# Kernel optimization log

Measured on AMD Instinct MI355X. Metric: run time of the kernel, lower is better.

## Reference

```python
import jax, jax.numpy as jnp
import numpy as np

K = 32  # k-th nearest neighbor (excluding self), matches KDistanceDetector(k=32)


def setup_inputs() -> dict:
    key = jax.random.key(0)
    B, D = 16384, 128
    images = jax.random.normal(key, (B, D), dtype=jnp.float32)
    return {"images": images}


def reference(images):
    # model is identity: vision_features = images, shape [B, D]
    x = images
    # torch.cdist p=2 with mm path: sq dists via gram matrix
    sq_norms = jnp.sum(x * x, axis=1)                      # [B]
    sq = sq_norms[:, None] + sq_norms[None, :] - 2.0 * (x @ x.T)  # [B, B]
    sq = jnp.maximum(sq, 0.0)
    B = x.shape[0]
    # Mask out the diagonal (self-distance). Original removes it and views
    # [B, B-1]; setting it to +inf before sorting yields the identical k-th
    # smallest value (inf sorts last), and keeps sqrt grads clean.
    diag = jnp.eye(B, dtype=bool)
    sq = jnp.where(diag, jnp.inf, sq)
    d = jnp.sqrt(sq)                                       # [B, B]
    a = jnp.sort(d, axis=1)                                # full per-row sort, as in original
    return a[:, K]                                         # [B]
```

## Files before the change

kernel.cpp:

```cpp
#include <hip/hip_runtime.h>


typedef unsigned short u16;
typedef unsigned int   u32;
typedef __attribute__((ext_vector_type(8))) u16    ushort8;
typedef __attribute__((ext_vector_type(8))) __bf16 bf16x8;
typedef __attribute__((ext_vector_type(4))) float  f32x4;
typedef __attribute__((ext_vector_type(4))) u32    u32x4;

#define NB   16384
#define ND   128
#define NSEG 32
#define SCAP 12
#define NTH  33
#define ZWH  (-2.62f)
#define NEGF (-3.0e38f)
#define POSF ( 3.0e38f)

#define OFF_X    ((size_t)0)
#define OFF_NORM (OFF_X    + (size_t)NB * ND * 2)
#define OFF_TACC (OFF_NORM + (size_t)NB * 4)
#define OFF_XBAR (OFF_TACC + (size_t)NB * 4)
#define OFF_SCAL (OFF_XBAR + 512)
#define OFF_CNTS (OFF_SCAL + 256)
#define OFF_CAND (OFF_CNTS + (size_t)NB * NSEG * 4)

static __device__ __forceinline__ u16 f2bf(float f) {
  u32 u = __float_as_uint(f);
  u32 r = u + 0x7FFFu + ((u >> 16) & 1u);
  return (u16)(r >> 16);
}
static __device__ __forceinline__ float bf2f(u16 h) {
  return __uint_as_float(((u32)h) << 16);
}

#if defined(__has_builtin)
#if __has_builtin(__builtin_amdgcn_global_load_lds)
#define HAVE_GLDS 1
#endif
#endif

static __device__ __forceinline__ void stage16(const u16* gsrc_lane,
                                               u16* lds_base, int l) {
#ifdef HAVE_GLDS
  __builtin_amdgcn_global_load_lds(
      (const __attribute__((address_space(1))) void*)gsrc_lane,
      (__attribute__((address_space(3))) void*)lds_base, 16, 0, 0);
#else
  *(ushort8*)(lds_base + l * 8) = *(const ushort8*)gsrc_lane;
#endif
}
static __device__ __forceinline__ void stage4(const float* gsrc_lane,
                                              float* lds_base, int l) {
#ifdef HAVE_GLDS
  __builtin_amdgcn_global_load_lds(
      (const __attribute__((address_space(1))) void*)gsrc_lane,
      (__attribute__((address_space(3))) void*)lds_base, 4, 0, 0);
#else
  lds_base[l] = *gsrc_lane;
#endif
}

__global__ void k_prep(const float* __restrict__ x, u16* __restrict__ X,
                       float* __restrict__ norms, float* xbar, float* scal) {
  if (blockIdx.x == 0) {
    int tt = threadIdx.x;
    if (tt < 128) xbar[tt] = 0.f;
    if (tt < 2)   scal[tt] = 0.f;
  }
  int w = threadIdx.x >> 6, l = threadIdx.x & 63;
  int r = blockIdx.x * 4 + w;
  const float2* xr2 = (const float2*)(x + (size_t)r * ND);
  float2 a = xr2[l];
  u16 h0 = f2bf(a.x), h1 = f2bf(a.y);
  float b0 = bf2f(h0), b1 = bf2f(h1);
  float n = b0 * b0 + b1 * b1;
#pragma unroll
  for (int off = 1; off < 64; off <<= 1) n += __shfl_xor(n, off, 64);
  *(u32*)(X + (size_t)r * ND + 2 * l) = (u32)h0 | ((u32)h1 << 16);
  if (l == 0) norms[r] = n;
}

__global__ void k_stats(const u16* __restrict__ X, const float* __restrict__ norms,
                        float* xbar, float* scal) {
  __shared__ float xs[16][128];
  __shared__ float red1[256], red2[256];
  int t = threadIdx.x;
  int cg = t & 15;
  int rs = t >> 4;
  int rbase = blockIdx.x * 256;
  float s[8] = {0.f, 0.f, 0.f, 0.f, 0.f, 0.f, 0.f, 0.f};
  for (int rr = 0; rr < 16; ++rr) {
    int row = rbase + rs + rr * 16;
    ushort8 v = *(const ushort8*)(X + (size_t)row * ND + cg * 8);
#pragma unroll
    for (int u = 0; u < 8; ++u) s[u] += bf2f(v[u]);
  }
#pragma unroll
  for (int u = 0; u < 8; ++u) xs[rs][cg * 8 + u] = s[u];
  float ln = norms[rbase + t];
  red1[t] = ln; red2[t] = ln * ln;
  __syncthreads();
  if (t < 128) {
    float a = 0.f;
    for (int rsub = 0; rsub < 16; ++rsub) a += xs[rsub][t];
    atomicAdd(&xbar[t], a);
  }
  for (int st = 128; st > 0; st >>= 1) {
    if (t < st) { red1[t] += red1[t + st]; red2[t] += red2[t + st]; }
    __syncthreads();
  }
  if (t == 0) { atomicAdd(&scal[0], red1[0]); atomicAdd(&scal[1], red2[0]); }
}

__global__ void k_thresh(const u16* __restrict__ X, const float* __restrict__ norms,
                         const float* __restrict__ xbar, const float* __restrict__ scal,
                         float* __restrict__ tacc) {
  __shared__ float xb[128];
  int t = threadIdx.x;
  if (t < 128) xb[t] = xbar[t] * (1.0f / NB);
  __syncthreads();
  int r = blockIdx.x * 256 + t;
  float n = norms[r];
  const u16* xr = X + (size_t)r * ND;
  float dot = 0.f;
#pragma unroll
  for (int c8 = 0; c8 < 16; ++c8) {
    ushort8 v = *(const ushort8*)(xr + c8 * 8);
#pragma unroll
    for (int j = 0; j < 8; ++j) dot += bf2f(v[j]) * xb[c8 * 8 + j];
  }
  float nbar = scal[0] * (1.0f / NB);
  float Vn = fmaxf(scal[1] * (1.0f / NB) - nbar * nbar, 0.f);
  float m = n + nbar - 2.f * dot;
  float v = Vn + 4.f * n * (nbar / ND);
  float nu = 2.f * m * m / v;
  float cc = v / (2.f * m);
  float a1 = 2.f / (9.f * nu);
  float inner = 1.f - a1 + ZWH * sqrtf(a1);
  float tsq = cc * nu * inner * inner * inner;
  tacc[r] = 0.5f * (n - tsq);
}

__global__ __launch_bounds__(256, 2) void k_gram(
    const u16* __restrict__ X, const float* __restrict__ norms,
    const float* __restrict__ tacc, u32* __restrict__ counts,
    float* __restrict__ cands) {
  __shared__ u16 ldsA[2][32 * 512];
  __shared__ __align__(16) float nchs[2][128];
  const int bid = blockIdx.x;
  const int logical = (bid & 7) * 64 + (bid >> 3);
  const int q = logical >> 7, strip = logical & 127;
  const int r0 = strip * 128;
  const int t = threadIdx.x, w = t >> 6, l = t & 63;
  const int wr = w & 1, wc = w >> 1;
  const int lm = l & 15, lq = l >> 4;
  const int koff = lq * 8;

  bf16x8 bfrag[4][4];
#pragma unroll
  for (int k = 0; k < 4; ++k)
#pragma unroll
    for (int j = 0; j < 4; ++j)
      bfrag[k][j] = __builtin_bit_cast(bf16x8, *(const ushort8*)(
          X + (size_t)(r0 + (wr * 4 + j) * 16 + lm) * ND + k * 32 + koff));

  int rj[4]; float tj[4]; u32 cnt4[4]; u32 segb[4];
#pragma unroll
  for (int j = 0; j < 4; ++j) {
    rj[j] = r0 + (wr * 4 + j) * 16 + lm;
    tj[j] = tacc[rj[j]];
    cnt4[j] = 0;
    segb[j] = (u32)(rj[j] * NSEG + q * 8 + wc * 4 + lq) * SCAP;
  }

  {
    const int c0 = q * 4096;
#pragma unroll
    for (int s = 0; s < 8; ++s) {
      int g = w * 8 + s;
      stage16(X + (size_t)(c0 + (g & 7) * 16 + lm) * ND + (g >> 3) * 32 + koff,
              &ldsA[0][g * 512], l);
    }
    if (w < 2) stage4(norms + c0 + w * 64 + l, &nchs[0][w * 64], l);
  }
  __syncthreads();

  for (int it = 0; it < 32; ++it) {
    const int cur = it & 1;
    const int c0 = q * 4096 + it * 128;
    if (it + 1 < 32) {
      const int c1 = c0 + 128;
      u16* dstA = ldsA[cur ^ 1];
#pragma unroll
      for (int s = 0; s < 8; ++s) {
        int g = w * 8 + s;
        stage16(X + (size_t)(c1 + (g & 7) * 16 + lm) * ND + (g >> 3) * 32 + koff,
                &dstA[g * 512], l);
      }
      if (w < 2) stage4(norms + c1 + w * 64 + l, &nchs[cur ^ 1][w * 64], l);
    }
    __builtin_amdgcn_sched_barrier(0);

    f32x4 acc[4][4];
#pragma unroll
    for (int i = 0; i < 4; ++i)
#pragma unroll
      for (int j = 0; j < 4; ++j) acc[i][j] = (f32x4){0.f, 0.f, 0.f, 0.f};

    const u16* srcA = ldsA[cur];
#pragma unroll
    for (int k = 0; k < 4; ++k) {
      bf16x8 af[4];
#pragma unroll
      for (int i = 0; i < 4; ++i)
        af[i] = __builtin_bit_cast(bf16x8,
                 *(const ushort8*)(&srcA[(k * 8 + wc * 4 + i) * 512 + l * 8]));
#pragma unroll
      for (int i = 0; i < 4; ++i)
#pragma unroll
        for (int j = 0; j < 4; ++j)
          acc[i][j] = __builtin_amdgcn_mfma_f32_16x16x32_bf16(af[i], bfrag[k][j], acc[i][j], 0, 0, 0);
    }

    f32x4 nch4[4];
#pragma unroll
    for (int i = 0; i < 4; ++i) {
      nch4[i] = *(const f32x4*)(&nchs[cur][wc * 64 + i * 16 + lq * 4]);
      nch4[i] = nch4[i] * 0.5f;
    }

    const bool dg = (c0 == r0);
#pragma unroll
    for (int i = 0; i < 4; ++i) {
#pragma unroll
      for (int j = 0; j < 4; ++j) {
        f32x4 val = acc[i][j] - nch4[i];
        float g01 = fmaxf(val[0], val[1]);
        float g23 = fmaxf(val[2], val[3]);
        if (fmaxf(g01, g23) >= tj[j]) {
#pragma unroll
          for (int v = 0; v < 4; ++v) {
            bool p = (val[v] >= tj[j]);
            if (dg) p = p && ((c0 + wc * 64 + i * 16 + lq * 4 + v) != rj[j]);
            if (p) {
              u32 c = cnt4[j];
              if (c < SCAP) cands[segb[j] + c] = val[v];
              cnt4[j] = c + 1;
            }
          }
        }
      }
    }

    __syncthreads();
  }
#pragma unroll
  for (int j = 0; j < 4; ++j)
    counts[rj[j] * NSEG + q * 8 + wc * 4 + lq] = cnt4[j];
}

__global__ void k_select(const u32* __restrict__ counts, const float* __restrict__ cands,
                         const float* __restrict__ norms, float* __restrict__ out) {
  int w = threadIdx.x >> 6, l = threadIdx.x & 63;
  int r = blockIdx.x * 4 + w;
  u32 myc = (l < NSEG) ? counts[r * NSEG + l] : 0u;
  u32 tot = myc, mx = myc;
#pragma unroll
  for (int off = 1; off < 64; off <<= 1) {
    tot += __shfl_xor(tot, off, 64);
    u32 o = (u32)__shfl_xor((int)mx, off, 64);
    mx = mx > o ? mx : o;
  }
  if (tot < NTH || mx > SCAP) return;

  const float* base = cands + (size_t)r * (NSEG * SCAP);
  float v0, v1, v2, v3, v4, v5;
#define LOADV(e, dst)                                        \
  {                                                          \
    int f = l + 64 * e;                                      \
    int sg = f / SCAP, sl = f - sg * SCAP;                   \
    u32 c = (u32)__shfl((int)myc, sg, 64);                   \
    float x = base[f];                                       \
    dst = (sl < (int)c) ? x : NEGF;                          \
  }
  LOADV(0, v0) LOADV(1, v1) LOADV(2, v2) LOADV(3, v3) LOADV(4, v4) LOADV(5, v5)
#undef LOADV

  float last = NEGF;
  for (int e = 0; e < NTH; ++e) {
    float m = fmaxf(fmaxf(fmaxf(v0, v1), fmaxf(v2, v3)), fmaxf(v4, v5));
#pragma unroll
    for (int off = 1; off < 64; off <<= 1) m = fmaxf(m, __shfl_xor(m, off, 64));
    bool mine = (v0 == m) || (v1 == m) || (v2 == m) || (v3 == m) || (v4 == m) || (v5 == m);
    unsigned long long bal = __ballot(mine);
    int owner = __ffsll(bal) - 1;
    if (l == owner) {
      if      (v0 == m) v0 = NEGF;
      else if (v1 == m) v1 = NEGF;
      else if (v2 == m) v2 = NEGF;
      else if (v3 == m) v3 = NEGF;
      else if (v4 == m) v4 = NEGF;
      else              v5 = NEGF;
    }
    last = m;
  }
  out[r] = sqrtf(fmaxf(norms[r] - 2.f * last, 0.f));
}

__global__ void k_fallback(const u32* __restrict__ counts, const u16* __restrict__ X,
                           const float* __restrict__ norms, float* __restrict__ out) {
  __shared__ float sq[NB];
  __shared__ float xr[ND];
  __shared__ float rmin[256];
  __shared__ int   ridx[256];
  __shared__ float tmin[256];
  __shared__ int   tidx[256];
  __shared__ int   nbad;
  __shared__ int   badlist[256];
  int t = threadIdx.x;
  if (t == 0) nbad = 0;
  __syncthreads();
  int r = blockIdx.x * 256 + t;
  u32 tot = 0, mx = 0;
#pragma unroll
  for (int s4 = 0; s4 < 8; ++s4) {
    u32x4 c = *(const u32x4*)(counts + (size_t)r * NSEG + s4 * 4);
#pragma unroll
    for (int u = 0; u < 4; ++u) { tot += c[u]; mx = c[u] > mx ? c[u] : mx; }
  }
  if (tot < NTH || mx > SCAP) { int p = atomicAdd(&nbad, 1); badlist[p] = r; }
  __syncthreads();
  int nb = nbad;
  for (int ii = 0; ii < nb; ++ii) {
    int rr = badlist[ii];
    if (t < 128) xr[t] = bf2f(X[(size_t)rr * ND + t]);
    __syncthreads();
    float n_r = norms[rr];
    for (int jj = 0; jj < 64; ++jj) {
      int j = t + 256 * jj;
      const u16* xj = X + (size_t)j * ND;
      float dot = 0.f;
#pragma unroll
      for (int c8 = 0; c8 < 16; ++c8) {
        ushort8 vv = *(const ushort8*)(xj + c8 * 8);
#pragma unroll
        for (int u = 0; u < 8; ++u) dot += bf2f(vv[u]) * xr[c8 * 8 + u];
      }
      sq[j] = (j == rr) ? POSF : fmaxf(n_r + norms[j] - 2.f * dot, 0.f);
    }
    __syncthreads();
    {
      float lmv = POSF; int lix = -1;
      for (int jj = 0; jj < 64; ++jj) {
        int j = t + 256 * jj;
        float s = sq[j];
        if (s < lmv) { lmv = s; lix = j; }
      }
      rmin[t] = lmv; ridx[t] = lix;
    }
    __syncthreads();
    float last = 0.f;
    for (int e = 0; e < NTH; ++e) {
      tmin[t] = rmin[t]; tidx[t] = ridx[t];
      __syncthreads();
      for (int s = 128; s > 0; s >>= 1) {
        if (t < s && tmin[t + s] < tmin[t]) { tmin[t] = tmin[t + s]; tidx[t] = tidx[t + s]; }
        __syncthreads();
      }
      float gm = tmin[0]; int gi = tidx[0];
      last = gm;
      __syncthreads();
      if (t == (gi & 255)) {
        sq[gi] = POSF;
        float lmv = POSF; int lix = -1;
        for (int jj = 0; jj < 64; ++jj) {
          int j = t + 256 * jj;
          float s = sq[j];
          if (s < lmv) { lmv = s; lix = j; }
        }
        rmin[t] = lmv; ridx[t] = lix;
      }
      __syncthreads();
    }
    if (t == 0) out[rr] = sqrtf(fmaxf(last, 0.f));
    __syncthreads();
  }
}

extern "C" void kernel_launch(void* const* d_in, const int* in_sizes, int n_in,
                              void* d_out, int out_size, void* d_ws, size_t ws_size,
                              hipStream_t stream) {
  const float* x = (const float*)d_in[0];
  float* out = (float*)d_out;
  char* ws = (char*)d_ws;
  u16*   X     = (u16*)  (ws + OFF_X);
  float* norms = (float*)(ws + OFF_NORM);
  float* tacc  = (float*)(ws + OFF_TACC);
  float* xbar  = (float*)(ws + OFF_XBAR);
  float* scal  = (float*)(ws + OFF_SCAL);
  u32*   cnts  = (u32*)  (ws + OFF_CNTS);
  float* cands = (float*)(ws + OFF_CAND);

  k_prep    <<<4096, 256, 0, stream>>>(x, X, norms, xbar, scal);
  k_stats   <<<64,   256, 0, stream>>>(X, norms, xbar, scal);
  k_thresh  <<<64,   256, 0, stream>>>(X, norms, xbar, scal, tacc);
  k_gram    <<<512,  256, 0, stream>>>(X, norms, tacc, cnts, cands);
  k_select  <<<4096, 256, 0, stream>>>(cnts, cands, norms, out);
  k_fallback<<<64,   256, 0, stream>>>(cnts, X, norms, out);
}
```

Before: 215.2 us.

## Fuse prep and stats kernels, replace atomics with per-block partials, nontemporal stores

Merges the bf16 conversion/norm kernel with the column-mean and norm-statistics kernel, so the input is read once and one launch is removed. The global atomics are replaced by per-block partial sums that the threshold kernel reduces itself, which also drops the zero-initialisation step. In the gram epilogue, the per-quad max early-out is removed and candidate and count writes become nontemporal stores. In exchange, each threshold block now re-reduces 256 partial rows, and without the early-out every element is compared individually.

Measured after the change: 211.2 us. About the same (-1.8%).

```diff
diff --git a/kernel.cpp b/kernel.cpp
--- a/kernel.cpp
+++ b/kernel.cpp
@@ -16,13 +16,14 @@
 #define ZWH  (-2.62f)
 #define NEGF (-3.0e38f)
 #define POSF ( 3.0e38f)
+#define NPB  64
+#define NPBL 256
 
 #define OFF_X    ((size_t)0)
 #define OFF_NORM (OFF_X    + (size_t)NB * ND * 2)
 #define OFF_TACC (OFF_NORM + (size_t)NB * 4)
-#define OFF_XBAR (OFF_TACC + (size_t)NB * 4)
-#define OFF_SCAL (OFF_XBAR + 512)
-#define OFF_CNTS (OFF_SCAL + 256)
+#define OFF_PART (OFF_TACC + (size_t)NB * 4)
+#define OFF_CNTS (OFF_PART + (size_t)NPBL * 130 * 4)
 #define OFF_CAND (OFF_CNTS + (size_t)NB * NSEG * 4)
 
 static __device__ __forceinline__ u16 f2bf(float f) {
@@ -61,64 +62,71 @@
 #endif
 }
 
-__global__ void k_prep(const float* __restrict__ x, u16* __restrict__ X,
-                       float* __restrict__ norms, float* xbar, float* scal) {
-  if (blockIdx.x == 0) {
-    int tt = threadIdx.x;
-    if (tt < 128) xbar[tt] = 0.f;
-    if (tt < 2)   scal[tt] = 0.f;
-  }
-  int w = threadIdx.x >> 6, l = threadIdx.x & 63;
-  int r = blockIdx.x * 4 + w;
-  const float2* xr2 = (const float2*)(x + (size_t)r * ND);
-  float2 a = xr2[l];
-  u16 h0 = f2bf(a.x), h1 = f2bf(a.y);
-  float b0 = bf2f(h0), b1 = bf2f(h1);
-  float n = b0 * b0 + b1 * b1;
-#pragma unroll
-  for (int off = 1; off < 64; off <<= 1) n += __shfl_xor(n, off, 64);
-  *(u32*)(X + (size_t)r * ND + 2 * l) = (u32)h0 | ((u32)h1 << 16);
-  if (l == 0) norms[r] = n;
-}
-
-__global__ void k_stats(const u16* __restrict__ X, const float* __restrict__ norms,
-                        float* xbar, float* scal) {
+__global__ void k_prepstats(const float* __restrict__ x, u16* __restrict__ X,
+                            float* __restrict__ norms, float* __restrict__ partial) {
   __shared__ float xs[16][128];
   __shared__ float red1[256], red2[256];
   int t = threadIdx.x;
   int cg = t & 15;
   int rs = t >> 4;
-  int rbase = blockIdx.x * 256;
-  float s[8] = {0.f, 0.f, 0.f, 0.f, 0.f, 0.f, 0.f, 0.f};
-  for (int rr = 0; rr < 16; ++rr) {
+  int rbase = blockIdx.x * NPB;
+  float cs[8] = {0.f, 0.f, 0.f, 0.f, 0.f, 0.f, 0.f, 0.f};
+  float s1 = 0.f, s2 = 0.f;
+#pragma unroll
+  for (int rr = 0; rr < NPB / 16; ++rr) {
     int row = rbase + rs + rr * 16;
-    ushort8 v = *(const ushort8*)(X + (size_t)row * ND + cg * 8);
-#pragma unroll
-    for (int u = 0; u < 8; ++u) s[u] += bf2f(v[u]);
-  }
-#pragma unroll
-  for (int u = 0; u < 8; ++u) xs[rs][cg * 8 + u] = s[u];
-  float ln = norms[rbase + t];
-  red1[t] = ln; red2[t] = ln * ln;
+    const float* src = x + (size_t)row * ND + cg * 8;
+    float4 a0 = *(const float4*)(src);
+    float4 a1 = *(const float4*)(src + 4);
+    float v[8] = {a0.x, a0.y, a0.z, a0.w, a1.x, a1.y, a1.z, a1.w};
+    ushort8 pack;
+    float ns = 0.f;
+#pragma unroll
+    for (int u = 0; u < 8; ++u) {
+      u16 h = f2bf(v[u]);
+      float b = bf2f(h);
+      pack[u] = h;
+      ns += b * b;
+      cs[u] += b;
+    }
+    *(ushort8*)(X + (size_t)row * ND + cg * 8) = pack;
+#pragma unroll
+    for (int off = 1; off < 16; off <<= 1) ns += __shfl_xor(ns, off, 64);
+    if (cg == 0) { norms[row] = ns; s1 += ns; s2 += ns * ns; }
+  }
+#pragma unroll
+  for (int u = 0; u < 8; ++u) xs[rs][cg * 8 + u] = cs[u];
+  red1[t] = s1; red2[t] = s2;
   __syncthreads();
   if (t < 128) {
     float a = 0.f;
-    for (int rsub = 0; rsub < 16; ++rsub) a += xs[rsub][t];
-    atomicAdd(&xbar[t], a);
+    for (int r2 = 0; r2 < 16; ++r2) a += xs[r2][t];
+    partial[(size_t)blockIdx.x * 130 + t] = a;
   }
   for (int st = 128; st > 0; st >>= 1) {
     if (t < st) { red1[t] += red1[t + st]; red2[t] += red2[t + st]; }
     __syncthreads();
   }
-  if (t == 0) { atomicAdd(&scal[0], red1[0]); atomicAdd(&scal[1], red2[0]); }
+  if (t == 0) {
+    partial[(size_t)blockIdx.x * 130 + 128] = red1[0];
+    partial[(size_t)blockIdx.x * 130 + 129] = red2[0];
+  }
 }
 
 __global__ void k_thresh(const u16* __restrict__ X, const float* __restrict__ norms,
-                         const float* __restrict__ xbar, const float* __restrict__ scal,
-                         float* __restrict__ tacc) {
+                         const float* __restrict__ partial, float* __restrict__ tacc) {
   __shared__ float xb[128];
+  __shared__ float ssum[2];
   int t = threadIdx.x;
-  if (t < 128) xb[t] = xbar[t] * (1.0f / NB);
+  if (t < 128) {
+    float a = 0.f;
+    for (int b = 0; b < NPBL; ++b) a += partial[(size_t)b * 130 + t];
+    xb[t] = a * (1.0f / NB);
+  } else if (t == 128 || t == 129) {
+    float a = 0.f;
+    for (int b = 0; b < NPBL; ++b) a += partial[(size_t)b * 130 + t];
+    ssum[t - 128] = a;
+  }
   __syncthreads();
   int r = blockIdx.x * 256 + t;
   float n = norms[r];
@@ -130,8 +138,8 @@
 #pragma unroll
     for (int j = 0; j < 8; ++j) dot += bf2f(v[j]) * xb[c8 * 8 + j];
   }
-  float nbar = scal[0] * (1.0f / NB);
-  float Vn = fmaxf(scal[1] * (1.0f / NB) - nbar * nbar, 0.f);
+  float nbar = ssum[0] * (1.0f / NB);
+  float Vn = fmaxf(ssum[1] * (1.0f / NB) - nbar * nbar, 0.f);
   float m = n + nbar - 2.f * dot;
   float v = Vn + 4.f * n * (nbar / ND);
   float nu = 2.f * m * m / v;
@@ -235,19 +243,16 @@
     for (int i = 0; i < 4; ++i) {
 #pragma unroll
       for (int j = 0; j < 4; ++j) {
-        f32x4 val = acc[i][j] - nch4[i];
-        float g01 = fmaxf(val[0], val[1]);
-        float g23 = fmaxf(val[2], val[3]);
-        if (fmaxf(g01, g23) >= tj[j]) {
-#pragma unroll
-          for (int v = 0; v < 4; ++v) {
-            bool p = (val[v] >= tj[j]);
-            if (dg) p = p && ((c0 + wc * 64 + i * 16 + lq * 4 + v) != rj[j]);
-            if (p) {
-              u32 c = cnt4[j];
-              if (c < SCAP) cands[segb[j] + c] = val[v];
-              cnt4[j] = c + 1;
-            }
+#pragma unroll
+        for (int v = 0; v < 4; ++v) {
+          float val = acc[i][j][v] - nch4[i][v];
+          bool p = (val >= tj[j]);
+          if (dg) p = p && ((c0 + wc * 64 + i * 16 + lq * 4 + v) != rj[j]);
+          if (p) {
+            u32 c = cnt4[j];
+            if (c < SCAP)
+              __builtin_nontemporal_store(val, &cands[segb[j] + c]);
+            cnt4[j] = c + 1;
           }
         }
       }
@@ -257,7 +262,7 @@
   }
 #pragma unroll
   for (int j = 0; j < 4; ++j)
-    counts[rj[j] * NSEG + q * 8 + wc * 4 + lq] = cnt4[j];
+    __builtin_nontemporal_store(cnt4[j], &counts[rj[j] * NSEG + q * 8 + wc * 4 + lq]);
 }
 
 __global__ void k_select(const u32* __restrict__ counts, const float* __restrict__ cands,
@@ -397,15 +402,13 @@
   u16*   X     = (u16*)  (ws + OFF_X);
   float* norms = (float*)(ws + OFF_NORM);
   float* tacc  = (float*)(ws + OFF_TACC);
-  float* xbar  = (float*)(ws + OFF_XBAR);
-  float* scal  = (float*)(ws + OFF_SCAL);
+  float* part  = (float*)(ws + OFF_PART);
   u32*   cnts  = (u32*)  (ws + OFF_CNTS);
   float* cands = (float*)(ws + OFF_CAND);
 
-  k_prep    <<<4096, 256, 0, stream>>>(x, X, norms, xbar, scal);
-  k_stats   <<<64,   256, 0, stream>>>(X, norms, xbar, scal);
-  k_thresh  <<<64,   256, 0, stream>>>(X, norms, xbar, scal, tacc);
-  k_gram    <<<512,  256, 0, stream>>>(X, norms, tacc, cnts, cands);
-  k_select  <<<4096, 256, 0, stream>>>(cnts, cands, norms, out);
-  k_fallback<<<64,   256, 0, stream>>>(cnts, X, norms, out);
-}
+  k_prepstats<<<NPBL, 256, 0, stream>>>(x, X, norms, part);
+  k_thresh   <<<64,   256, 0, stream>>>(X, norms, part, tacc);
+  k_gram     <<<512,  256, 0, stream>>>(X, norms, tacc, cnts, cands);
+  k_select   <<<4096, 256, 0, stream>>>(cnts, cands, norms, out);
+  k_fallback <<<64,   256, 0, stream>>>(cnts, X, norms, out);
+}
```
